# Kernel tuning notes

Hardware: AMD Instinct MI355X
Metric: run time of the kernel (lower is better)

The kernel has to match this reference:

```python
import jax, jax.numpy as jnp
import numpy as np

BN_EPS = 1e-5
KEEP_RATIO = 0.25
MIN_TOPK = 4


def setup_inputs() -> dict:
    key = jax.random.key(0)
    ks = jax.random.split(key, 8)
    B, C, H, W, HID = 32, 768, 32, 32, 96
    x = jax.random.normal(ks[0], (B, C, H, W), dtype=jnp.float32)
    # fan-in scaled weights so score magnitudes stay sane for softmax
    w1 = jax.random.normal(ks[1], (HID, C, 1, 1), dtype=jnp.float32) / np.sqrt(C)
    bn_gamma = jax.random.uniform(ks[2], (HID,), dtype=jnp.float32) + 0.5
    bn_beta = jax.random.normal(ks[3], (HID,), dtype=jnp.float32) * 0.1
    bn_mean = jax.random.normal(ks[4], (HID,), dtype=jnp.float32) * 0.1
    bn_var = jax.random.uniform(ks[5], (HID,), dtype=jnp.float32) + 0.5
    w2 = jax.random.normal(ks[6], (1, HID, 3, 3), dtype=jnp.float32) / np.sqrt(HID * 9)
    b2 = jax.random.normal(ks[7], (1,), dtype=jnp.float32) * 0.1
    return {"x": x, "w1": w1, "bn_gamma": bn_gamma, "bn_beta": bn_beta,
            "bn_mean": bn_mean, "bn_var": bn_var, "w2": w2, "b2": b2}


def reference(x, w1, bn_gamma, bn_beta, bn_mean, bn_var, w2, b2):
    B, C, H, W = x.shape
    N = H * W
    # 1x1 conv (no bias) as channel contraction: [B,C,H,W] x [HID,C] -> [B,HID,H,W]
    h = jnp.einsum('bchw,oc->bohw', x, w1[:, :, 0, 0])
    # BatchNorm in inference mode (running stats)
    scale = (bn_gamma / jnp.sqrt(bn_var + BN_EPS))[None, :, None, None]
    h = h * scale + (bn_beta - bn_mean * bn_gamma / jnp.sqrt(bn_var + BN_EPS))[None, :, None, None]
    h = jax.nn.relu(h)
    # 3x3 conv HID -> 1, padding=1
    score = jax.lax.conv_general_dilated(
        h, w2, window_strides=(1, 1), padding='SAME',
        dimension_numbers=('NCHW', 'OIHW', 'NCHW')) + b2[None, :, None, None]
    s = score.reshape(B, N)
    K = min(max(MIN_TOPK, int(N * KEEP_RATIO)), N)
    top_vals, top_idx = jax.lax.top_k(s, K)  # [B,K] (sorted; weighted sum is order-invariant)
    x_flat = x.reshape(B, C, N)
    sel = jnp.take_along_axis(x_flat, top_idx[:, None, :], axis=2)  # [B,C,K]
    w = jax.nn.softmax(top_vals, axis=1)[:, None, :]               # [B,1,K]
    v = jnp.sum(sel * w, axis=2)                                    # [B,C]
    # dropout p=0.0 -> identity
    return v, score.reshape(B, 1, H, W)
```

## Files before the change

kernel.cpp:

```cpp
#include <hip/hip_runtime.h>
#include <math.h>

#define BB 32
#define CC 768
#define HID 96
#define NPIX 1024
#define KSEL 256
#define BN_EPS_F 1e-5f

typedef __bf16 bf16x8 __attribute__((ext_vector_type(8)));
typedef float f32x4 __attribute__((ext_vector_type(4)));

__device__ __forceinline__ unsigned short f2bf(float f) {
    unsigned u = __float_as_uint(f);
    return (unsigned short)((u + 0x7FFFu + ((u >> 16) & 1u)) >> 16);
}
__device__ __forceinline__ unsigned pack2(float lo, float hi) {
    return (unsigned)f2bf(lo) | ((unsigned)f2bf(hi) << 16);
}

__global__ __launch_bounds__(256) void k0_prep(
    const float* __restrict__ w1, const float* __restrict__ gamma,
    const float* __restrict__ beta, const float* __restrict__ mean,
    const float* __restrict__ var,
    unsigned short* __restrict__ w1b, float* __restrict__ scale,
    float* __restrict__ shift)
{
    int t = threadIdx.x, bk = blockIdx.x;
    if (bk < 72) {
        int idx = (bk * 256 + t) * 4;
        float4 v = *reinterpret_cast<const float4*>(w1 + idx);
        uint2 o;
        o.x = pack2(v.x, v.y);
        o.y = pack2(v.z, v.w);
        *reinterpret_cast<uint2*>(w1b + idx) = o;
    } else if (t < HID) {
        float sc = gamma[t] * rsqrtf(var[t] + BN_EPS_F);
        scale[t] = sc;
        shift[t] = beta[t] - mean[t] * sc;
    }
}

__global__ __launch_bounds__(256) void k1_gemm_mfma(
    const float* __restrict__ x, const unsigned short* __restrict__ w1b,
    const float* __restrict__ scale, const float* __restrict__ shift,
    float* __restrict__ h_out)
{
    __shared__ unsigned short W1s[96][72];
    __shared__ unsigned Xs[32][68];
    __shared__ float sc_s[HID], sh_s[HID];

    const int t = threadIdx.x;
    const int b = blockIdx.y;
    const int n0 = blockIdx.x * 64;
    const int wave = t >> 6, lane = t & 63;
    const int lm = lane & 15, g = lane >> 4;
    const int nl = wave * 16 + lm;

    if (t < HID) { sc_s[t] = scale[t]; sh_s[t] = shift[t]; }

    f32x4 acc[6];
#pragma unroll
    for (int mt = 0; mt < 6; ++mt) acc[mt] = (f32x4){0.f, 0.f, 0.f, 0.f};

    const int kp = t >> 3, q = t & 7;
    const float* xbase = x + ((size_t)b * CC) * NPIX + n0;

    for (int c0 = 0; c0 < CC; c0 += 64) {
        __syncthreads();
        {
            const float* r0 = xbase + (size_t)(c0 + 2 * kp) * NPIX;
            const float* r1 = r0 + NPIX;
#pragma unroll
            for (int i2 = 0; i2 < 2; ++i2) {
                int noff = q * 4 + i2 * 32;
                float4 a4 = *reinterpret_cast<const float4*>(r0 + noff);
                float4 b4 = *reinterpret_cast<const float4*>(r1 + noff);
                uint4 pk;
                pk.x = pack2(a4.x, b4.x);
                pk.y = pack2(a4.y, b4.y);
                pk.z = pack2(a4.z, b4.z);
                pk.w = pack2(a4.w, b4.w);
                *reinterpret_cast<uint4*>(&Xs[kp][noff]) = pk;
            }
        }
#pragma unroll
        for (int i = 0; i < 3; ++i) {
            int idx = t + i * 256;
            int m = idx >> 3, ko = (idx & 7) * 8;
            uint4 wv = *reinterpret_cast<const uint4*>(w1b + (size_t)m * CC + c0 + ko);
            *reinterpret_cast<uint4*>(&W1s[m][ko]) = wv;
        }
        __syncthreads();

#pragma unroll
        for (int half = 0; half < 2; ++half) {
            uint4 bu;
            bu.x = Xs[16 * half + 4 * g + 0][nl];
            bu.y = Xs[16 * half + 4 * g + 1][nl];
            bu.z = Xs[16 * half + 4 * g + 2][nl];
            bu.w = Xs[16 * half + 4 * g + 3][nl];
            bf16x8 bfr = __builtin_bit_cast(bf16x8, bu);
#pragma unroll
            for (int mt = 0; mt < 6; ++mt) {
                uint4 au = *reinterpret_cast<const uint4*>(
                    &W1s[mt * 16 + lm][half * 32 + g * 8]);
                acc[mt] = __builtin_amdgcn_mfma_f32_16x16x32_bf16(
                    __builtin_bit_cast(bf16x8, au), bfr, acc[mt], 0, 0, 0);
            }
        }
    }

#pragma unroll
    for (int mt = 0; mt < 6; ++mt) {
#pragma unroll
        for (int r = 0; r < 4; ++r) {
            int o = mt * 16 + g * 4 + r;
            float v = fmaxf(acc[mt][r] * sc_s[o] + sh_s[o], 0.f);
            h_out[((size_t)b * HID + o) * NPIX + n0 + nl] = v;
        }
    }
}

__global__ __launch_bounds__(256) void k2_conv3x3(
    const float* __restrict__ h_in, const float* __restrict__ w2,
    const float* __restrict__ b2, float* __restrict__ score_out)
{
    __shared__ float hs[16][10][34];
    __shared__ float w2s[HID][9];

    const int t = threadIdx.x;
    const int ry = blockIdx.x, b = blockIdx.y;
    const int y = t >> 5, xx = t & 31;
    const int Y = ry * 8 + y;

    for (int i = t; i < 16 * 10 * 34; i += 256) ((float*)hs)[i] = 0.f;
    for (int i = t; i < HID * 9; i += 256) ((float*)w2s)[i] = w2[i];

    const float* hb = h_in + (size_t)b * HID * NPIX;
    float acc = 0.f;

    for (int c0 = 0; c0 < HID; c0 += 16) {
        __syncthreads();
#pragma unroll
        for (int i = 0; i < 20; ++i) {
            int idx = t + i * 256;
            int col = idx & 31, row = (idx >> 5) % 10, ch = idx / 320;
            int Ya = ry * 8 - 1 + row;
            if (Ya >= 0 && Ya < 32)
                hs[ch][row][col + 1] = hb[(size_t)(c0 + ch) * NPIX + Ya * 32 + col];
        }
        __syncthreads();
#pragma unroll
        for (int ch = 0; ch < 16; ++ch) {
            float s = 0.f;
#pragma unroll
            for (int ky = 0; ky < 3; ++ky)
#pragma unroll
                for (int kx = 0; kx < 3; ++kx)
                    s += hs[ch][y + ky][xx + kx] * w2s[c0 + ch][ky * 3 + kx];
            acc += s;
        }
    }
    score_out[b * NPIX + Y * 32 + xx] = acc + b2[0];
}

__global__ __launch_bounds__(256) void k3_topk_softmax(
    const float* __restrict__ score, float* __restrict__ weight)
{
    __shared__ unsigned hist[256];
    __shared__ unsigned wtot[4];
    __shared__ unsigned pcnt16[16];
    __shared__ float redf[4];
    __shared__ unsigned sh_bin, sh_rem;

    const int t = threadIdx.x, b = blockIdx.x;
    const int lane = t & 63, wv = t >> 6;

    float fvals[4];
    unsigned uvals[4];
#pragma unroll
    for (int i = 0; i < 4; ++i) {
        float f = score[b * NPIX + t + 256 * i];
        fvals[i] = f;
        unsigned u = __float_as_uint(f);
        uvals[i] = (u & 0x80000000u) ? ~u : (u | 0x80000000u);
    }

    unsigned prefix = 0, rem = KSEL;
    for (int p = 3; p >= 0; --p) {
        hist[t] = 0;
        __syncthreads();
        const int sh_hi = (p + 1) * 8;
#pragma unroll
        for (int i = 0; i < 4; ++i) {
            unsigned u = uvals[i];
            bool match = (p == 3) || ((u >> sh_hi) == (prefix >> sh_hi));
            if (match) atomicAdd(&hist[(u >> (p * 8)) & 0xffu], 1u);
        }
        __syncthreads();
        unsigned own = hist[t];
        unsigned val = own;
#pragma unroll
        for (int off = 1; off <= 32; off <<= 1) {
            unsigned o2 = __shfl_down(val, off);
            if (lane + off < 64) val += o2;
        }
        if (lane == 0) wtot[wv] = val;
        __syncthreads();
        unsigned suff = val;
        for (int w = wv + 1; w < 4; ++w) suff += wtot[w];
        unsigned nexts = suff - own;
        if (suff >= rem && nexts < rem) { sh_bin = (unsigned)t; sh_rem = rem - nexts; }
        __syncthreads();
        prefix |= (sh_bin << (p * 8));
        rem = sh_rem;
        __syncthreads();
    }
    const unsigned T = prefix, need = rem;

    float m = -INFINITY;
#pragma unroll
    for (int i = 0; i < 4; ++i) m = fmaxf(m, fvals[i]);
#pragma unroll
    for (int off = 32; off >= 1; off >>= 1) m = fmaxf(m, __shfl_xor(m, off));
    if (lane == 0) redf[wv] = m;
    __syncthreads();
    m = fmaxf(fmaxf(redf[0], redf[1]), fmaxf(redf[2], redf[3]));

    unsigned lp[4]; bool eqf[4], gtf[4];
    unsigned long long lmask = (1ULL << lane) - 1ULL;
#pragma unroll
    for (int i = 0; i < 4; ++i) {
        bool eq = (uvals[i] == T);
        eqf[i] = eq; gtf[i] = (uvals[i] > T);
        unsigned long long mk = __ballot(eq);
        lp[i] = (unsigned)__popcll(mk & lmask);
        if (lane == 0) pcnt16[i * 4 + wv] = (unsigned)__popcll(mk);
    }
    __syncthreads();
    unsigned cum = 0, baseArr[4];
#pragma unroll
    for (int ii = 0; ii < 4; ++ii) {
        unsigned b0 = cum;
        for (int w = 0; w < wv; ++w) b0 += pcnt16[ii * 4 + w];
        baseArr[ii] = b0;
        for (int w = 0; w < 4; ++w) cum += pcnt16[ii * 4 + w];
    }
    float evals[4], sumExp = 0.f;
#pragma unroll
    for (int i = 0; i < 4; ++i) {
        bool sel = gtf[i] || (eqf[i] && (baseArr[i] + lp[i]) < need);
        float e = sel ? expf(fvals[i] - m) : 0.f;
        evals[i] = e;
        sumExp += e;
    }
#pragma unroll
    for (int off = 32; off >= 1; off >>= 1) sumExp += __shfl_xor(sumExp, off);
    if (lane == 0) redf[wv] = sumExp;
    __syncthreads();
    float inv = 1.0f / (redf[0] + redf[1] + redf[2] + redf[3]);
#pragma unroll
    for (int i = 0; i < 4; ++i)
        weight[b * NPIX + i * 256 + t] = evals[i] * inv;
}

__global__ __launch_bounds__(256) void k4_weighted_sum(
    const float* __restrict__ x, const float* __restrict__ weight,
    float* __restrict__ v)
{
    __shared__ float wsm[NPIX];
    const int t = threadIdx.x;
    const int b = blockIdx.x / 192, cg = blockIdx.x % 192;

    *reinterpret_cast<float4*>(&wsm[t * 4]) =
        *reinterpret_cast<const float4*>(&weight[b * NPIX + t * 4]);
    __syncthreads();

    const int lane = t & 63, wvv = t >> 6;
    const int c = cg * 4 + wvv;
    const float* xr = x + ((size_t)b * CC + c) * NPIX;

    float acc = 0.f;
#pragma unroll
    for (int j = 0; j < 4; ++j) {
        int off = j * 256 + lane * 4;
        float4 xv = *reinterpret_cast<const float4*>(xr + off);
        float4 wv4 = *reinterpret_cast<const float4*>(&wsm[off]);
        acc += xv.x * wv4.x + xv.y * wv4.y + xv.z * wv4.z + xv.w * wv4.w;
    }
#pragma unroll
    for (int off = 32; off >= 1; off >>= 1) acc += __shfl_xor(acc, off);
    if (lane == 0) v[(size_t)b * CC + c] = acc;
}

extern "C" void kernel_launch(void* const* d_in, const int* in_sizes, int n_in,
                              void* d_out, int out_size, void* d_ws, size_t ws_size,
                              hipStream_t stream)
{
    const float* x     = (const float*)d_in[0];
    const float* w1    = (const float*)d_in[1];
    const float* gamma = (const float*)d_in[2];
    const float* beta  = (const float*)d_in[3];
    const float* mean  = (const float*)d_in[4];
    const float* var   = (const float*)d_in[5];
    const float* w2    = (const float*)d_in[6];
    const float* b2    = (const float*)d_in[7];

    float* out   = (float*)d_out;
    float* vout  = out;
    float* score = out + BB * CC;

    float* h       = (float*)d_ws;
    float* weight  = h + (size_t)BB * HID * NPIX;
    unsigned short* w1b = (unsigned short*)(weight + BB * NPIX);
    float* scale   = (float*)(w1b + HID * CC);
    float* shift   = scale + HID;

    k0_prep<<<73, 256, 0, stream>>>(w1, gamma, beta, mean, var, w1b, scale, shift);
    k1_gemm_mfma<<<dim3(16, BB), 256, 0, stream>>>(x, w1b, scale, shift, h);
    k2_conv3x3<<<dim3(4, BB), 256, 0, stream>>>(h, w2, b2, score);
    k3_topk_softmax<<<BB, 256, 0, stream>>>(score, weight);
    k4_weighted_sum<<<BB * (CC / 4), 256, 0, stream>>>(x, weight, vout);
}
```

Baseline: 91.23 us.

## Double-buffer X tiles in GEMM and fuse conv3x3 with top-k softmax

The 1x1-conv GEMM now double-buffers the bf16-packed X tile in LDS. It prefetches the next 64-channel slab into registers while the current one is computed, so only one barrier is needed per iteration. W1 is no longer staged in LDS and is read straight from global memory, relying on caches. Separately, the 3x3 conv and the radix top-k/softmax are merged into one 1024-thread kernel per batch. This removes a launch and the score round-trip, at the cost of cutting conv parallelism from 128 blocks to 32 and using a larger LDS tile.

```diff
diff --git a/kernel.cpp b/kernel.cpp
--- a/kernel.cpp
+++ b/kernel.cpp
@@ -46,8 +46,7 @@
     const float* __restrict__ scale, const float* __restrict__ shift,
     float* __restrict__ h_out)
 {
-    __shared__ unsigned short W1s[96][72];
-    __shared__ unsigned Xs[32][68];
+    __shared__ unsigned Xs[2][32][68];
     __shared__ float sc_s[HID], sh_s[HID];
 
     const int t = threadIdx.x;
@@ -56,6 +55,7 @@
     const int wave = t >> 6, lane = t & 63;
     const int lm = lane & 15, g = lane >> 4;
     const int nl = wave * 16 + lm;
+    const int kp = t >> 3, q = t & 7;
 
     if (t < HID) { sc_s[t] = scale[t]; sh_s[t] = shift[t]; }
 
@@ -63,52 +63,64 @@
 #pragma unroll
     for (int mt = 0; mt < 6; ++mt) acc[mt] = (f32x4){0.f, 0.f, 0.f, 0.f};
 
-    const int kp = t >> 3, q = t & 7;
     const float* xbase = x + ((size_t)b * CC) * NPIX + n0;
 
+    {
+        const float* r0 = xbase + (size_t)(2 * kp) * NPIX;
+        const float* r1 = r0 + NPIX;
+        float4 a0 = *reinterpret_cast<const float4*>(r0 + q * 4);
+        float4 a1 = *reinterpret_cast<const float4*>(r0 + q * 4 + 32);
+        float4 b0 = *reinterpret_cast<const float4*>(r1 + q * 4);
+        float4 b1 = *reinterpret_cast<const float4*>(r1 + q * 4 + 32);
+        uint4 p0, p1;
+        p0.x = pack2(a0.x, b0.x); p0.y = pack2(a0.y, b0.y);
+        p0.z = pack2(a0.z, b0.z); p0.w = pack2(a0.w, b0.w);
+        p1.x = pack2(a1.x, b1.x); p1.y = pack2(a1.y, b1.y);
+        p1.z = pack2(a1.z, b1.z); p1.w = pack2(a1.w, b1.w);
+        *reinterpret_cast<uint4*>(&Xs[0][kp][q * 4]) = p0;
+        *reinterpret_cast<uint4*>(&Xs[0][kp][q * 4 + 32]) = p1;
+    }
+    __syncthreads();
+
+    int cur = 0;
     for (int c0 = 0; c0 < CC; c0 += 64) {
-        __syncthreads();
-        {
-            const float* r0 = xbase + (size_t)(c0 + 2 * kp) * NPIX;
+        const bool hasNext = (c0 + 64 < CC);
+        float4 na0, na1, nb0, nb1;
+        if (hasNext) {
+            const float* r0 = xbase + (size_t)(c0 + 64 + 2 * kp) * NPIX;
             const float* r1 = r0 + NPIX;
-#pragma unroll
-            for (int i2 = 0; i2 < 2; ++i2) {
-                int noff = q * 4 + i2 * 32;
-                float4 a4 = *reinterpret_cast<const float4*>(r0 + noff);
-                float4 b4 = *reinterpret_cast<const float4*>(r1 + noff);
-                uint4 pk;
-                pk.x = pack2(a4.x, b4.x);
-                pk.y = pack2(a4.y, b4.y);
-                pk.z = pack2(a4.z, b4.z);
-                pk.w = pack2(a4.w, b4.w);
-                *reinterpret_cast<uint4*>(&Xs[kp][noff]) = pk;
-            }
-        }
-#pragma unroll
-        for (int i = 0; i < 3; ++i) {
-            int idx = t + i * 256;
-            int m = idx >> 3, ko = (idx & 7) * 8;
-            uint4 wv = *reinterpret_cast<const uint4*>(w1b + (size_t)m * CC + c0 + ko);
-            *reinterpret_cast<uint4*>(&W1s[m][ko]) = wv;
-        }
-        __syncthreads();
-
+            na0 = *reinterpret_cast<const float4*>(r0 + q * 4);
+            na1 = *reinterpret_cast<const float4*>(r0 + q * 4 + 32);
+            nb0 = *reinterpret_cast<const float4*>(r1 + q * 4);
+            nb1 = *reinterpret_cast<const float4*>(r1 + q * 4 + 32);
+        }
 #pragma unroll
         for (int half = 0; half < 2; ++half) {
             uint4 bu;
-            bu.x = Xs[16 * half + 4 * g + 0][nl];
-            bu.y = Xs[16 * half + 4 * g + 1][nl];
-            bu.z = Xs[16 * half + 4 * g + 2][nl];
-            bu.w = Xs[16 * half + 4 * g + 3][nl];
+            bu.x = Xs[cur][16 * half + 4 * g + 0][nl];
+            bu.y = Xs[cur][16 * half + 4 * g + 1][nl];
+            bu.z = Xs[cur][16 * half + 4 * g + 2][nl];
+            bu.w = Xs[cur][16 * half + 4 * g + 3][nl];
             bf16x8 bfr = __builtin_bit_cast(bf16x8, bu);
 #pragma unroll
             for (int mt = 0; mt < 6; ++mt) {
                 uint4 au = *reinterpret_cast<const uint4*>(
-                    &W1s[mt * 16 + lm][half * 32 + g * 8]);
+                    w1b + (size_t)(mt * 16 + lm) * CC + c0 + half * 32 + g * 8);
                 acc[mt] = __builtin_amdgcn_mfma_f32_16x16x32_bf16(
                     __builtin_bit_cast(bf16x8, au), bfr, acc[mt], 0, 0, 0);
             }
         }
+        if (hasNext) {
+            uint4 p0, p1;
+            p0.x = pack2(na0.x, nb0.x); p0.y = pack2(na0.y, nb0.y);
+            p0.z = pack2(na0.z, nb0.z); p0.w = pack2(na0.w, nb0.w);
+            p1.x = pack2(na1.x, nb1.x); p1.y = pack2(na1.y, nb1.y);
+            p1.z = pack2(na1.z, nb1.z); p1.w = pack2(na1.w, nb1.w);
+            *reinterpret_cast<uint4*>(&Xs[cur ^ 1][kp][q * 4]) = p0;
+            *reinterpret_cast<uint4*>(&Xs[cur ^ 1][kp][q * 4 + 32]) = p1;
+        }
+        __syncthreads();
+        cur ^= 1;
     }
 
 #pragma unroll
@@ -122,20 +134,25 @@
     }
 }
 
-__global__ __launch_bounds__(256) void k2_conv3x3(
+__global__ __launch_bounds__(1024) void k23_conv_topk(
     const float* __restrict__ h_in, const float* __restrict__ w2,
-    const float* __restrict__ b2, float* __restrict__ score_out)
-{
-    __shared__ float hs[16][10][34];
-    __shared__ float w2s[HID][9];
-
-    const int t = threadIdx.x;
-    const int ry = blockIdx.x, b = blockIdx.y;
+    const float* __restrict__ b2, float* __restrict__ score_out,
+    float* __restrict__ weight)
+{
+    __shared__ float hs[16][34][34];
+    __shared__ float w2s[HID * 9];
+    __shared__ unsigned hist[256];
+    __shared__ unsigned wtot4[4];
+    __shared__ unsigned pcnt16[16];
+    __shared__ float redf16[16];
+    __shared__ unsigned sh_bin, sh_rem;
+
+    const int t = threadIdx.x, b = blockIdx.x;
+    const int lane = t & 63, wv = t >> 6;
     const int y = t >> 5, xx = t & 31;
-    const int Y = ry * 8 + y;
-
-    for (int i = t; i < 16 * 10 * 34; i += 256) ((float*)hs)[i] = 0.f;
-    for (int i = t; i < HID * 9; i += 256) ((float*)w2s)[i] = w2[i];
+
+    for (int i = t; i < 16 * 34 * 34; i += 1024) ((float*)hs)[i] = 0.f;
+    if (t < HID * 9) w2s[t] = w2[t];
 
     const float* hb = h_in + (size_t)b * HID * NPIX;
     float acc = 0.f;
@@ -143,12 +160,11 @@
     for (int c0 = 0; c0 < HID; c0 += 16) {
         __syncthreads();
 #pragma unroll
-        for (int i = 0; i < 20; ++i) {
-            int idx = t + i * 256;
-            int col = idx & 31, row = (idx >> 5) % 10, ch = idx / 320;
-            int Ya = ry * 8 - 1 + row;
-            if (Ya >= 0 && Ya < 32)
-                hs[ch][row][col + 1] = hb[(size_t)(c0 + ch) * NPIX + Ya * 32 + col];
+        for (int i = 0; i < 16; ++i) {
+            int idx = t + i * 1024;
+            int ch = idx >> 10, px = idx & 1023;
+            int row = px >> 5, col = px & 31;
+            hs[ch][row + 1][col + 1] = hb[(size_t)(c0 + ch) * NPIX + px];
         }
         __syncthreads();
 #pragma unroll
@@ -158,60 +174,43 @@
             for (int ky = 0; ky < 3; ++ky)
 #pragma unroll
                 for (int kx = 0; kx < 3; ++kx)
-                    s += hs[ch][y + ky][xx + kx] * w2s[c0 + ch][ky * 3 + kx];
+                    s += hs[ch][y + ky][xx + kx] * w2s[(c0 + ch) * 9 + ky * 3 + kx];
             acc += s;
         }
     }
-    score_out[b * NPIX + Y * 32 + xx] = acc + b2[0];
-}
-
-__global__ __launch_bounds__(256) void k3_topk_softmax(
-    const float* __restrict__ score, float* __restrict__ weight)
-{
-    __shared__ unsigned hist[256];
-    __shared__ unsigned wtot[4];
-    __shared__ unsigned pcnt16[16];
-    __shared__ float redf[4];
-    __shared__ unsigned sh_bin, sh_rem;
-
-    const int t = threadIdx.x, b = blockIdx.x;
-    const int lane = t & 63, wv = t >> 6;
-
-    float fvals[4];
-    unsigned uvals[4];
-#pragma unroll
-    for (int i = 0; i < 4; ++i) {
-        float f = score[b * NPIX + t + 256 * i];
-        fvals[i] = f;
-        unsigned u = __float_as_uint(f);
-        uvals[i] = (u & 0x80000000u) ? ~u : (u | 0x80000000u);
-    }
+    const float fval = acc + b2[0];
+    score_out[b * NPIX + t] = fval;
+
+    unsigned u = __float_as_uint(fval);
+    const unsigned uval = (u & 0x80000000u) ? ~u : (u | 0x80000000u);
 
     unsigned prefix = 0, rem = KSEL;
+    unsigned own, val;
     for (int p = 3; p >= 0; --p) {
-        hist[t] = 0;
+        if (t < 256) hist[t] = 0;
         __syncthreads();
         const int sh_hi = (p + 1) * 8;
-#pragma unroll
-        for (int i = 0; i < 4; ++i) {
-            unsigned u = uvals[i];
-            bool match = (p == 3) || ((u >> sh_hi) == (prefix >> sh_hi));
-            if (match) atomicAdd(&hist[(u >> (p * 8)) & 0xffu], 1u);
-        }
-        __syncthreads();
-        unsigned own = hist[t];
-        unsigned val = own;
-#pragma unroll
-        for (int off = 1; off <= 32; off <<= 1) {
-            unsigned o2 = __shfl_down(val, off);
-            if (lane + off < 64) val += o2;
-        }
-        if (lane == 0) wtot[wv] = val;
-        __syncthreads();
-        unsigned suff = val;
-        for (int w = wv + 1; w < 4; ++w) suff += wtot[w];
-        unsigned nexts = suff - own;
-        if (suff >= rem && nexts < rem) { sh_bin = (unsigned)t; sh_rem = rem - nexts; }
+        bool match = (p == 3) || ((uval >> sh_hi) == (prefix >> sh_hi));
+        if (match) atomicAdd(&hist[(uval >> (p * 8)) & 0xffu], 1u);
+        __syncthreads();
+        own = 0; val = 0;
+        if (t < 256) {
+            own = hist[t];
+            val = own;
+#pragma unroll
+            for (int off = 1; off <= 32; off <<= 1) {
+                unsigned o2 = __shfl_down(val, off);
+                if (lane + off < 64) val += o2;
+            }
+            if (lane == 0) wtot4[wv] = val;
+        }
+        __syncthreads();
+        if (t < 256) {
+            unsigned suff = val;
+            for (int w = wv + 1; w < 4; ++w) suff += wtot4[w];
+            unsigned nexts = suff - own;
+            if (suff >= rem && nexts < rem) { sh_bin = (unsigned)t; sh_rem = rem - nexts; }
+        }
         __syncthreads();
         prefix |= (sh_bin << (p * 8));
         rem = sh_rem;
@@ -219,50 +218,34 @@
     }
     const unsigned T = prefix, need = rem;
 
-    float m = -INFINITY;
-#pragma unroll
-    for (int i = 0; i < 4; ++i) m = fmaxf(m, fvals[i]);
+    float m = fval;
 #pragma unroll
     for (int off = 32; off >= 1; off >>= 1) m = fmaxf(m, __shfl_xor(m, off));
-    if (lane == 0) redf[wv] = m;
-    __syncthreads();
-    m = fmaxf(fmaxf(redf[0], redf[1]), fmaxf(redf[2], redf[3]));
-
-    unsigned lp[4]; bool eqf[4], gtf[4];
-    unsigned long long lmask = (1ULL << lane) - 1ULL;
-#pragma unroll
-    for (int i = 0; i < 4; ++i) {
-        bool eq = (uvals[i] == T);
-        eqf[i] = eq; gtf[i] = (uvals[i] > T);
-        unsigned long long mk = __ballot(eq);
-        lp[i] = (unsigned)__popcll(mk & lmask);
-        if (lane == 0) pcnt16[i * 4 + wv] = (unsigned)__popcll(mk);
-    }
-    __syncthreads();
-    unsigned cum = 0, baseArr[4];
-#pragma unroll
-    for (int ii = 0; ii < 4; ++ii) {
-        unsigned b0 = cum;
-        for (int w = 0; w < wv; ++w) b0 += pcnt16[ii * 4 + w];
-        baseArr[ii] = b0;
-        for (int w = 0; w < 4; ++w) cum += pcnt16[ii * 4 + w];
-    }
-    float evals[4], sumExp = 0.f;
-#pragma unroll
-    for (int i = 0; i < 4; ++i) {
-        bool sel = gtf[i] || (eqf[i] && (baseArr[i] + lp[i]) < need);
-        float e = sel ? expf(fvals[i] - m) : 0.f;
-        evals[i] = e;
-        sumExp += e;
-    }
+    if (lane == 0) redf16[wv] = m;
+    __syncthreads();
+#pragma unroll
+    for (int w = 0; w < 16; ++w) m = fmaxf(m, redf16[w]);
+
+    bool eq = (uval == T), gt = (uval > T);
+    unsigned long long mk = __ballot(eq);
+    unsigned lp = (unsigned)__popcll(mk & ((1ULL << lane) - 1ULL));
+    if (lane == 0) pcnt16[wv] = (unsigned)__popcll(mk);
+    __syncthreads();
+    unsigned rank = lp;
+    for (int w = 0; w < wv; ++w) rank += pcnt16[w];
+    bool sel = gt || (eq && rank < need);
+    float e = sel ? expf(fval - m) : 0.f;
+
+    float sumExp = e;
 #pragma unroll
     for (int off = 32; off >= 1; off >>= 1) sumExp += __shfl_xor(sumExp, off);
-    if (lane == 0) redf[wv] = sumExp;
-    __syncthreads();
-    float inv = 1.0f / (redf[0] + redf[1] + redf[2] + redf[3]);
-#pragma unroll
-    for (int i = 0; i < 4; ++i)
-        weight[b * NPIX + i * 256 + t] = evals[i] * inv;
+    if (lane == 0) redf16[wv] = sumExp;
+    __syncthreads();
+    float tot = 0.f;
+#pragma unroll
+    for (int w = 0; w < 16; ++w) tot += redf16[w];
+
+    weight[b * NPIX + t] = e * (1.0f / tot);
 }
 
 __global__ __launch_bounds__(256) void k4_weighted_sum(
@@ -319,7 +302,6 @@
 
     k0_prep<<<73, 256, 0, stream>>>(w1, gamma, beta, mean, var, w1b, scale, shift);
     k1_gemm_mfma<<<dim3(16, BB), 256, 0, stream>>>(x, w1b, scale, shift, h);
-    k2_conv3x3<<<dim3(4, BB), 256, 0, stream>>>(h, w2, b2, score);
-    k3_topk_softmax<<<BB, 256, 0, stream>>>(score, weight);
+    k23_conv_topk<<<BB, 1024, 0, stream>>>(h, w2, b2, score, weight);
     k4_weighted_sum<<<BB * (CC / 4), 256, 0, stream>>>(x, weight, vout);
 }
```

Result: slower. 136.9 us (+50.1%).

## Double-buffer GEMM tiles with register prefetch and retile conv3x3 blocks

Applied to the files above, without the earlier changes.

The 1x1-conv GEMM kernel now covers 128 pixels per block, two N-subtiles per wave, and reuses each loaded W1 fragment across both. It double-buffers the X and W1 shared-memory tiles, prefetching the next channel chunk into registers while MFMAs run on the current one, which drops one barrier per iteration. The 3x3 conv kernel moves to 128-thread blocks of 4 rows each, with float4 global loads into a padded shared tile and explicit zeroing of only the halo columns. The GEMM grid is halved (256 blocks), which may reduce occupancy and latency hiding, and register pressure rises.

```diff
diff --git a/kernel.cpp b/kernel.cpp
--- a/kernel.cpp
+++ b/kernel.cpp
@@ -46,109 +46,162 @@
     const float* __restrict__ scale, const float* __restrict__ shift,
     float* __restrict__ h_out)
 {
-    __shared__ unsigned short W1s[96][72];
-    __shared__ unsigned Xs[32][68];
+    __shared__ unsigned Xs[2][32][132];
+    __shared__ unsigned short W1s[2][96][72];
     __shared__ float sc_s[HID], sh_s[HID];
 
     const int t = threadIdx.x;
     const int b = blockIdx.y;
-    const int n0 = blockIdx.x * 64;
+    const int n0 = blockIdx.x * 128;
     const int wave = t >> 6, lane = t & 63;
     const int lm = lane & 15, g = lane >> 4;
-    const int nl = wave * 16 + lm;
+    const int kp = t >> 3, q = t & 7;
 
     if (t < HID) { sc_s[t] = scale[t]; sh_s[t] = shift[t]; }
 
-    f32x4 acc[6];
-#pragma unroll
-    for (int mt = 0; mt < 6; ++mt) acc[mt] = (f32x4){0.f, 0.f, 0.f, 0.f};
-
-    const int kp = t >> 3, q = t & 7;
-    const float* xbase = x + ((size_t)b * CC) * NPIX + n0;
-
-    for (int c0 = 0; c0 < CC; c0 += 64) {
-        __syncthreads();
-        {
-            const float* r0 = xbase + (size_t)(c0 + 2 * kp) * NPIX;
-            const float* r1 = r0 + NPIX;
-#pragma unroll
-            for (int i2 = 0; i2 < 2; ++i2) {
-                int noff = q * 4 + i2 * 32;
-                float4 a4 = *reinterpret_cast<const float4*>(r0 + noff);
-                float4 b4 = *reinterpret_cast<const float4*>(r1 + noff);
-                uint4 pk;
-                pk.x = pack2(a4.x, b4.x);
-                pk.y = pack2(a4.y, b4.y);
-                pk.z = pack2(a4.z, b4.z);
-                pk.w = pack2(a4.w, b4.w);
-                *reinterpret_cast<uint4*>(&Xs[kp][noff]) = pk;
-            }
+    f32x4 acc[6][2];
+#pragma unroll
+    for (int mt = 0; mt < 6; ++mt)
+#pragma unroll
+        for (int ns = 0; ns < 2; ++ns) acc[mt][ns] = (f32x4){0.f, 0.f, 0.f, 0.f};
+
+    const float* xbase = x + (size_t)b * CC * NPIX + n0;
+
+    {
+        const float* r0 = xbase + (size_t)(2 * kp) * NPIX;
+        const float* r1 = r0 + NPIX;
+#pragma unroll
+        for (int j = 0; j < 4; ++j) {
+            int nc = q * 16 + 4 * j;
+            float4 a4 = *reinterpret_cast<const float4*>(r0 + nc);
+            float4 b4 = *reinterpret_cast<const float4*>(r1 + nc);
+            uint4 pk;
+            pk.x = pack2(a4.x, b4.x); pk.y = pack2(a4.y, b4.y);
+            pk.z = pack2(a4.z, b4.z); pk.w = pack2(a4.w, b4.w);
+            *reinterpret_cast<uint4*>(&Xs[0][kp][nc]) = pk;
         }
 #pragma unroll
         for (int i = 0; i < 3; ++i) {
             int idx = t + i * 256;
             int m = idx >> 3, ko = (idx & 7) * 8;
-            uint4 wv = *reinterpret_cast<const uint4*>(w1b + (size_t)m * CC + c0 + ko);
-            *reinterpret_cast<uint4*>(&W1s[m][ko]) = wv;
-        }
-        __syncthreads();
-
+            uint4 wv = *reinterpret_cast<const uint4*>(w1b + (size_t)m * CC + ko);
+            *reinterpret_cast<uint4*>(&W1s[0][m][ko]) = wv;
+        }
+    }
+    __syncthreads();
+
+    int cur = 0;
+    for (int c0 = 0; c0 < CC; c0 += 64) {
+        const bool hasNext = (c0 + 64 < CC);
+        float4 xa[4], xb[4];
+        uint4 wreg[3];
+        if (hasNext) {
+            const float* r0 = xbase + (size_t)(c0 + 64 + 2 * kp) * NPIX;
+            const float* r1 = r0 + NPIX;
+#pragma unroll
+            for (int j = 0; j < 4; ++j) {
+                int nc = q * 16 + 4 * j;
+                xa[j] = *reinterpret_cast<const float4*>(r0 + nc);
+                xb[j] = *reinterpret_cast<const float4*>(r1 + nc);
+            }
+#pragma unroll
+            for (int i = 0; i < 3; ++i) {
+                int idx = t + i * 256;
+                int m = idx >> 3, ko = (idx & 7) * 8;
+                wreg[i] = *reinterpret_cast<const uint4*>(
+                    w1b + (size_t)m * CC + c0 + 64 + ko);
+            }
+        }
 #pragma unroll
         for (int half = 0; half < 2; ++half) {
-            uint4 bu;
-            bu.x = Xs[16 * half + 4 * g + 0][nl];
-            bu.y = Xs[16 * half + 4 * g + 1][nl];
-            bu.z = Xs[16 * half + 4 * g + 2][nl];
-            bu.w = Xs[16 * half + 4 * g + 3][nl];
-            bf16x8 bfr = __builtin_bit_cast(bf16x8, bu);
-#pragma unroll
-            for (int mt = 0; mt < 6; ++mt) {
-                uint4 au = *reinterpret_cast<const uint4*>(
-                    &W1s[mt * 16 + lm][half * 32 + g * 8]);
-                acc[mt] = __builtin_amdgcn_mfma_f32_16x16x32_bf16(
-                    __builtin_bit_cast(bf16x8, au), bfr, acc[mt], 0, 0, 0);
-            }
-        }
-    }
-
-#pragma unroll
-    for (int mt = 0; mt < 6; ++mt) {
-#pragma unroll
-        for (int r = 0; r < 4; ++r) {
-            int o = mt * 16 + g * 4 + r;
-            float v = fmaxf(acc[mt][r] * sc_s[o] + sh_s[o], 0.f);
-            h_out[((size_t)b * HID + o) * NPIX + n0 + nl] = v;
-        }
-    }
-}
-
-__global__ __launch_bounds__(256) void k2_conv3x3(
+            uint4 au[6];
+#pragma unroll
+            for (int mt = 0; mt < 6; ++mt)
+                au[mt] = *reinterpret_cast<const uint4*>(
+                    &W1s[cur][mt * 16 + lm][half * 32 + g * 8]);
+#pragma unroll
+            for (int ns = 0; ns < 2; ++ns) {
+                int nl = wave * 32 + ns * 16 + lm;
+                uint4 bu;
+                bu.x = Xs[cur][16 * half + 4 * g + 0][nl];
+                bu.y = Xs[cur][16 * half + 4 * g + 1][nl];
+                bu.z = Xs[cur][16 * half + 4 * g + 2][nl];
+                bu.w = Xs[cur][16 * half + 4 * g + 3][nl];
+                bf16x8 bfr = __builtin_bit_cast(bf16x8, bu);
+#pragma unroll
+                for (int mt = 0; mt < 6; ++mt)
+                    acc[mt][ns] = __builtin_amdgcn_mfma_f32_16x16x32_bf16(
+                        __builtin_bit_cast(bf16x8, au[mt]), bfr, acc[mt][ns], 0, 0, 0);
+            }
+        }
+        if (hasNext) {
+#pragma unroll
+            for (int j = 0; j < 4; ++j) {
+                int nc = q * 16 + 4 * j;
+                uint4 pk;
+                pk.x = pack2(xa[j].x, xb[j].x); pk.y = pack2(xa[j].y, xb[j].y);
+                pk.z = pack2(xa[j].z, xb[j].z); pk.w = pack2(xa[j].w, xb[j].w);
+                *reinterpret_cast<uint4*>(&Xs[cur ^ 1][kp][nc]) = pk;
+            }
+#pragma unroll
+            for (int i = 0; i < 3; ++i) {
+                int idx = t + i * 256;
+                int m = idx >> 3, ko = (idx & 7) * 8;
+                *reinterpret_cast<uint4*>(&W1s[cur ^ 1][m][ko]) = wreg[i];
+            }
+        }
+        __syncthreads();
+        cur ^= 1;
+    }
+
+#pragma unroll
+    for (int mt = 0; mt < 6; ++mt)
+#pragma unroll
+        for (int ns = 0; ns < 2; ++ns) {
+#pragma unroll
+            for (int r = 0; r < 4; ++r) {
+                int o = mt * 16 + g * 4 + r;
+                int n = n0 + wave * 32 + ns * 16 + lm;
+                float v = fmaxf(acc[mt][ns][r] * sc_s[o] + sh_s[o], 0.f);
+                h_out[((size_t)b * HID + o) * NPIX + n] = v;
+            }
+        }
+}
+
+__global__ __launch_bounds__(128) void k2_conv3x3(
     const float* __restrict__ h_in, const float* __restrict__ w2,
     const float* __restrict__ b2, float* __restrict__ score_out)
 {
-    __shared__ float hs[16][10][34];
-    __shared__ float w2s[HID][9];
+    __shared__ float hs[16][6][40];
+    __shared__ float w2s[HID * 9];
 
     const int t = threadIdx.x;
-    const int ry = blockIdx.x, b = blockIdx.y;
+    const int ytile = blockIdx.x, b = blockIdx.y;
     const int y = t >> 5, xx = t & 31;
-    const int Y = ry * 8 + y;
-
-    for (int i = t; i < 16 * 10 * 34; i += 256) ((float*)hs)[i] = 0.f;
-    for (int i = t; i < HID * 9; i += 256) ((float*)w2s)[i] = w2[i];
+    const int Y = ytile * 4 + y;
+
+    for (int i = t; i < HID * 9; i += 128) w2s[i] = w2[i];
 
     const float* hb = h_in + (size_t)b * HID * NPIX;
     float acc = 0.f;
 
     for (int c0 = 0; c0 < HID; c0 += 16) {
         __syncthreads();
-#pragma unroll
-        for (int i = 0; i < 20; ++i) {
-            int idx = t + i * 256;
-            int col = idx & 31, row = (idx >> 5) % 10, ch = idx / 320;
-            int Ya = ry * 8 - 1 + row;
-            if (Ya >= 0 && Ya < 32)
-                hs[ch][row][col + 1] = hb[(size_t)(c0 + ch) * NPIX + Ya * 32 + col];
+        for (int i = t; i < 192; i += 128) {
+            int ch = i / 12, rr = (i % 12) >> 1, col = (i & 1) ? 36 : 3;
+            hs[ch][rr][col] = 0.f;
+        }
+#pragma unroll
+        for (int i = 0; i < 6; ++i) {
+            int idx = t + i * 128;
+            int ch = idx / 48, rem = idx % 48;
+            int rr = rem >> 3, qq = rem & 7;
+            int gy = ytile * 4 - 1 + rr;
+            float4 v = (gy >= 0 && gy < 32)
+                ? *reinterpret_cast<const float4*>(
+                      hb + (size_t)(c0 + ch) * NPIX + gy * 32 + qq * 4)
+                : (float4){0.f, 0.f, 0.f, 0.f};
+            *reinterpret_cast<float4*>(&hs[ch][rr][4 + qq * 4]) = v;
         }
         __syncthreads();
 #pragma unroll
@@ -158,7 +211,7 @@
             for (int ky = 0; ky < 3; ++ky)
 #pragma unroll
                 for (int kx = 0; kx < 3; ++kx)
-                    s += hs[ch][y + ky][xx + kx] * w2s[c0 + ch][ky * 3 + kx];
+                    s += hs[ch][y + ky][3 + xx + kx] * w2s[(c0 + ch) * 9 + ky * 3 + kx];
             acc += s;
         }
     }
@@ -318,8 +371,8 @@
     float* shift   = scale + HID;
 
     k0_prep<<<73, 256, 0, stream>>>(w1, gamma, beta, mean, var, w1b, scale, shift);
-    k1_gemm_mfma<<<dim3(16, BB), 256, 0, stream>>>(x, w1b, scale, shift, h);
-    k2_conv3x3<<<dim3(4, BB), 256, 0, stream>>>(h, w2, b2, score);
+    k1_gemm_mfma<<<dim3(8, BB), 256, 0, stream>>>(x, w1b, scale, shift, h);
+    k2_conv3x3<<<dim3(8, BB), 128, 0, stream>>>(h, w2, b2, score);
     k3_topk_softmax<<<BB, 256, 0, stream>>>(score, weight);
     k4_weighted_sum<<<BB * (CC / 4), 256, 0, stream>>>(x, weight, vout);
 }
```

New measurement: 91.26 us. About the same (+0.0%).
